# Performance work log

Hardware: AMD Instinct MI355X
Metric: run time of the kernel (lower is better)

The kernel has to match this reference:

```python
import jax, jax.numpy as jnp
import numpy as np

N_SUBJECTS = 16
N_LABELS = 8
DENS_TEMP = 0.1  # args.ProtoSim_dens_temp


def setup_inputs() -> dict:
    key = jax.random.key(0)
    k1, k2, k3 = jax.random.split(key, 3)
    B, C, D = 16384, 2, 1024
    X_data = jax.random.normal(k1, (B, C, D), dtype=jnp.float32)
    subject = jax.random.randint(k2, (B,), 0, N_SUBJECTS, dtype=jnp.int64) if jax.config.jax_enable_x64 else jax.random.randint(k2, (B,), 0, N_SUBJECTS).astype(jnp.int32)
    labels = jax.random.randint(k3, (B,), 0, N_LABELS).astype(subject.dtype)
    return {"X_data": X_data, "subject": subject, "labels": labels}


def reference(X_data, subject, labels):
    B, C, D = X_data.shape
    K = N_SUBJECTS * N_LABELS  # all (subject,label) groups assumed present
    # contrast_feature = cat(unbind(X_data, 1), 0) -> [B*C, D]
    feat = X_data.swapaxes(0, 1).reshape(B * C, D)
    sub2 = jnp.tile(subject, C)          # cat((subject, subject))
    lab2 = jnp.tile(labels, C)
    # torch.unique sorts -> group g = subject * N_LABELS + label matches loop order
    gid = sub2 * N_LABELS + lab2
    counts = jax.ops.segment_sum(jnp.ones((B * C,), feat.dtype), gid, num_segments=K)  # (K,)
    centroid = jax.ops.segment_sum(feat, gid, num_segments=K) / counts[:, None]       # (K, D)
    # per-row euclidean distance to own group centroid (torch.cdist to 1 point)
    dist = jnp.linalg.norm(feat - centroid[gid], axis=1)                               # (B*C,)
    mean_sqrt = jax.ops.segment_sum(jnp.sqrt(dist), gid, num_segments=K) / counts
    density = mean_sqrt / jnp.log(counts + 10.0)
    density = jnp.where(counts <= 1.0, density.max(), density)
    density = jnp.clip(density, jnp.quantile(density, 0.1), jnp.quantile(density, 0.9))
    density = DENS_TEMP * density / density.mean()                                     # (K,)
    # masks: positives = same label, different subject
    g_sub = jnp.arange(K) // N_LABELS
    g_lab = jnp.arange(K) % N_LABELS
    subj_mask = (sub2[:, None] != g_sub[None, :]).astype(feat.dtype)  # (B*C, K)
    lab_mask = (lab2[:, None] == g_lab[None, :]).astype(feat.dtype)
    mask = subj_mask * lab_mask
    # every row has N_SUBJECTS-1 positives (all groups present), so no row filtering
    sim = (feat @ centroid.T) / density[None, :]                                        # (B*C, K)
    sim = sim - sim.max(axis=1, keepdims=True)
    pos = sim * mask
    logp = jax.nn.log_softmax(pos, axis=1)
    row_loss = -(mask * logp).sum(axis=1) / mask.sum(axis=1)  # soft-target CE / #pos
    return row_loss.reshape(C, B).mean()
```

## Files before the change

### kernel.cpp

```cpp
#include <hip/hip_runtime.h>
#include <hip/hip_bf16.h>
#include <math.h>

#define NSUB 16
#define NLAB 8
#define KG 128
#define BN 16384
#define DD 1024

typedef float v4f __attribute__((ext_vector_type(4)));
typedef short short8v __attribute__((ext_vector_type(8)));
typedef unsigned short ushort4v __attribute__((ext_vector_type(4)));

static __device__ __forceinline__ short f2bf(float f) {
    unsigned u = __builtin_bit_cast(unsigned, f);
    unsigned r = (u + 0x7fffu + ((u >> 16) & 1u)) >> 16;
    return (short)r;
}

static __device__ __forceinline__ float bf2f(unsigned short u) {
    unsigned v = ((unsigned)u) << 16;
    return __builtin_bit_cast(float, v);
}

static __device__ __forceinline__ unsigned packbf2(float x, float y) {
    union { __hip_bfloat162 h; unsigned u; } c;
    c.h = __float22bfloat162_rn(float2{x, y});
    return c.u;
}

__global__ __launch_bounds__(1024) void k0_gid(const int* __restrict__ subject,
                                               const int* __restrict__ labels,
                                               int* __restrict__ gid, int* __restrict__ hist) {
    __shared__ int h[KG];
    int t = threadIdx.x;
    if (t < KG) h[t] = 0;
    __syncthreads();
    int b = blockIdx.x * 1024 + t;
    int g = subject[b] * NLAB + labels[b];
    gid[b] = g;
    atomicAdd(&h[g], 1);
    __syncthreads();
    if (t < KG) hist[blockIdx.x * KG + t] = h[t];
}

__global__ __launch_bounds__(1024) void k0c_scatter(const int* __restrict__ gid,
                                                    const int* __restrict__ hist,
                                                    int* __restrict__ cnt,
                                                    int* __restrict__ rowlist) {
    __shared__ int tots[KG], base0[KG], lcur[KG];
    int t = threadIdx.x, bi = blockIdx.x;
    if (t < KG) {
        int tot = 0, pre = 0;
#pragma unroll
        for (int j = 0; j < 16; ++j) {
            int v = hist[j * KG + t];
            tot += v;
            if (j < bi) pre += v;
        }
        tots[t] = tot;
        base0[t] = pre;
        lcur[t] = 0;
        if (bi == 0) cnt[t] = tot;
    }
    __syncthreads();
    if (t < KG) {
        int o = 0;
        for (int j = 0; j < t; ++j) o += tots[j];
        base0[t] += o;
    }
    __syncthreads();
    int b = bi * 1024 + t;
    int g = gid[b];
    rowlist[base0[g] + atomicAdd(&lcur[g], 1)] = b;
}

__global__ __launch_bounds__(256) void k1g_part(const float* __restrict__ X,
                                                const int* __restrict__ rowlist,
                                                const int* __restrict__ cnt,
                                                float* __restrict__ part2) {
    int g = blockIdx.x >> 3;
    int half = (blockIdx.x >> 2) & 1;
    int chunk = blockIdx.x & 3;
    int t = threadIdx.x, lane = t & 63, w = t >> 6;
    int c = t >> 7, td = t & 127;
    __shared__ int rows[512];
    __shared__ int sh_no[2];
    __shared__ float acc4[256][4];
    if (w == 0) {
        int v = 0;
        if (lane < g) v += cnt[lane];
        if (lane + 64 < g) v += cnt[lane + 64];
#pragma unroll
        for (int x = 32; x; x >>= 1) v += __shfl_xor(v, x, 64);
        if (lane == 0) { sh_no[0] = v; sh_no[1] = cnt[g]; }
    }
    __syncthreads();
    int o = sh_no[0], n = min(sh_no[1], 512);
    for (int i = t; i < n; i += 256) rows[i] = rowlist[o + i];
    __syncthreads();
    size_t coff = (size_t)c * 1024 + half * 512 + td * 4;
    float4 s4 = make_float4(0.f, 0.f, 0.f, 0.f);
    int i = chunk;
    for (; i + 28 < n; i += 32) {
        float4 v[8];
#pragma unroll
        for (int u = 0; u < 8; ++u)
            v[u] = *(const float4*)(X + (size_t)rows[i + 4 * u] * 2048 + coff);
#pragma unroll
        for (int u = 0; u < 8; ++u) {
            s4.x += v[u].x; s4.y += v[u].y; s4.z += v[u].z; s4.w += v[u].w;
        }
    }
    for (; i < n; i += 4) {
        float4 v = *(const float4*)(X + (size_t)rows[i] * 2048 + coff);
        s4.x += v.x; s4.y += v.y; s4.z += v.z; s4.w += v.w;
    }
    acc4[t][0] = s4.x; acc4[t][1] = s4.y; acc4[t][2] = s4.z; acc4[t][3] = s4.w;
    __syncthreads();
    if (t < 128) {
        float4 out;
        out.x = acc4[t][0] + acc4[t + 128][0];
        out.y = acc4[t][1] + acc4[t + 128][1];
        out.z = acc4[t][2] + acc4[t + 128][2];
        out.w = acc4[t][3] + acc4[t + 128][3];
        *(float4*)(part2 + (size_t)blockIdx.x * 512 + t * 4) = out;
    }
}

__global__ __launch_bounds__(256) void k1r2_reduce(const float* __restrict__ part2,
                                                   const int* __restrict__ cnt,
                                                   unsigned short* __restrict__ Btil,
                                                   float* __restrict__ cnormPart) {
    int g = blockIdx.x, t = threadIdx.x, lane = t & 63, w = t >> 6;
    __shared__ float wsum[4];
    int n = min(cnt[g], 512);
    int d0 = t * 4;
    int half = d0 >> 9, dloc = d0 & 511;
    const float* pp = part2 + ((size_t)g * 8 + half * 4) * 512 + dloc;
    float4 s4 = make_float4(0.f, 0.f, 0.f, 0.f);
#pragma unroll
    for (int chunk = 0; chunk < 4; ++chunk) {
        float4 v = *(const float4*)(pp + chunk * 512);
        s4.x += v.x; s4.y += v.y; s4.z += v.z; s4.w += v.w;
    }
    float inv = 1.f / (2.f * (float)n);
    float cx[4] = {s4.x * inv, s4.y * inv, s4.z * inv, s4.w * inv};
    int base_t = (d0 >> 5) * 512 + ((d0 >> 3) & 3) * 128 + (g & 15) * 8 + (d0 & 7);
    uint2 st;
    st.x = packbf2(cx[0], cx[1]);
    st.y = packbf2(cx[2], cx[3]);
    *(uint2*)(Btil + (size_t)(g >> 4) * 16384 + base_t) = st;
    float s = cx[0] * cx[0] + cx[1] * cx[1] + cx[2] * cx[2] + cx[3] * cx[3];
#pragma unroll
    for (int x = 32; x; x >>= 1) s += __shfl_xor(s, x, 64);
    if (lane == 0) wsum[w] = s;
    __syncthreads();
    if (t == 0) {
        cnormPart[g] = wsum[0] + wsum[1] + wsum[2] + wsum[3];
        cnormPart[KG + g] = 0.f;
    }
}

__global__ __launch_bounds__(256) void k2_tile(const float* __restrict__ X,
                                               unsigned short* __restrict__ Atil) {
    __shared__ unsigned lds[8192];
    int t = threadIdx.x, lane = t & 63, w = t >> 6;
    int rt = blockIdx.x;
#pragma unroll
    for (int p = 0; p < 4; ++p) {
        int m = w * 4 + p;
        int r = rt * 16 + m;
        const float* xp = X + (size_t)(r & (BN - 1)) * 2048 + (size_t)(r >> 14) * 1024;
        unsigned swz = (unsigned)((m & 7) << 2);
        unsigned mbase = (unsigned)m * 512;
#pragma unroll
        for (int j = 0; j < 4; ++j) {
            int d0 = j * 256 + lane * 4;
            float4 v = *(const float4*)(xp + d0);
            unsigned wi = mbase + (((unsigned)(d0 >> 1)) ^ swz);
            lds[wi] = packbf2(v.x, v.y);
            lds[wi + 1] = packbf2(v.z, v.w);
        }
    }
    __syncthreads();
    size_t gbase = (size_t)rt * 16384;
#pragma unroll
    for (int p = 0; p < 8; ++p) {
        int wo = p * 1024 + t * 4;
        int kc = wo >> 8;
        int q = (wo >> 6) & 3;
        int m = (wo >> 2) & 15;
        unsigned wi = (unsigned)m * 512 +
                      (((unsigned)(kc * 16 + q * 4)) ^ (unsigned)((m & 7) << 2));
        uint4 val = *(const uint4*)&lds[wi];
        *(uint4*)(Atil + gbase + (size_t)wo * 2) = val;
    }
}

__global__ __launch_bounds__(256) void k5a_dot(const unsigned short* __restrict__ Atil,
                                               const unsigned short* __restrict__ Btil,
                                               const int* __restrict__ gid,
                                               const float* __restrict__ cnormPart,
                                               unsigned short* __restrict__ Dotb,
                                               float* __restrict__ sqsPart) {
    __shared__ float h[KG];
    __shared__ float cnormS[KG];
    int t = threadIdx.x, lane = t & 63, w = t >> 6;
    if (t < KG) {
        h[t] = 0.f;
        cnormS[t] = cnormPart[t] + cnormPart[KG + t];
    }
    __syncthreads();
    int rt = blockIdx.x * 4 + w;
    int m = lane & 15, q = lane >> 4;
    const unsigned short* ap = Atil + (size_t)rt * 16384 + lane * 8;
    const unsigned short* bp = Btil + lane * 8;

    v4f acc[8];
#pragma unroll
    for (int j = 0; j < 8; ++j) acc[j] = (v4f){0.f, 0.f, 0.f, 0.f};

    short8v Af[2], Bf[2][8];
#pragma unroll
    for (int p = 0; p < 2; ++p) {
        Af[p] = *(const short8v*)(ap + p * 512);
#pragma unroll
        for (int gt = 0; gt < 8; ++gt)
            Bf[p][gt] = *(const short8v*)(bp + (size_t)gt * 16384 + p * 512);
    }
    float s0 = 0.f;
#pragma unroll
    for (int kc = 0; kc < 32; ++kc) {
        const int cur = kc & 1;
        short8v nA, nB[8];
        if (kc + 2 < 32) {
            nA = *(const short8v*)(ap + (kc + 2) * 512);
#pragma unroll
            for (int gt = 0; gt < 8; ++gt)
                nB[gt] = *(const short8v*)(bp + (size_t)gt * 16384 + (kc + 2) * 512);
        }
#pragma unroll
        for (int gt = 0; gt < 8; ++gt)
            acc[gt] = __builtin_amdgcn_mfma_f32_16x16x32_bf16(Af[cur], Bf[cur][gt], acc[gt], 0, 0, 0);
        {
            union { short8v s; unsigned u[4]; } ua;
            ua.s = Af[cur];
#pragma unroll
            for (int r = 0; r < 4; ++r) {
                float l0 = __builtin_bit_cast(float, ua.u[r] << 16);
                float h0 = __builtin_bit_cast(float, ua.u[r] & 0xffff0000u);
                s0 = fmaf(l0, l0, s0); s0 = fmaf(h0, h0, s0);
            }
        }
        if (kc + 2 < 32) {
            Af[cur] = nA;
#pragma unroll
            for (int gt = 0; gt < 8; ++gt) Bf[cur][gt] = nB[gt];
        }
    }

    s0 += __shfl_xor(s0, 16, 64); s0 += __shfl_xor(s0, 32, 64);

    int bid = blockIdx.x;
#pragma unroll
    for (int reg = 0; reg < 4; ++reg) {
        int rr = w * 16 + q * 4 + reg;
        int row = bid * 64 + rr;
        int b = row & (BN - 1);
        int g = gid[b];
        float own = 0.f;
#pragma unroll
        for (int gt = 0; gt < 8; ++gt) {
            float v = acc[gt][reg];
            size_t idx = (((size_t)bid * 32 + gt * 4 + (m >> 2)) * 64 + rr) * 4 + (m & 3);
            Dotb[idx] = (unsigned short)f2bf(v);
            if ((g >> 4) == gt) own = v;
        }
        float rn = __shfl(s0, q * 4 + reg, 64);
        if ((g & 15) == m) {
            float d2 = fmaxf(rn - 2.f * own + cnormS[g], 0.f);
            atomicAdd(&h[g], sqrtf(sqrtf(d2)));
        }
    }
    __syncthreads();
    if (t < KG) sqsPart[(size_t)blockIdx.x * KG + t] = h[t];
}

__global__ __launch_bounds__(128) void k5b_loss(const unsigned short* __restrict__ Dotb,
                                                const int* __restrict__ gid,
                                                const float* __restrict__ sqsPart,
                                                const int* __restrict__ cnt,
                                                float* __restrict__ out) {
    __shared__ float tmp[KG], d1s[KG], qv[4];
    __shared__ float recipDen[KG];
    __shared__ float wsum[2];
    int t = threadIdx.x;
    float cntf = 0.f, d0v = 0.f, v = 0.f;
    if (t < KG) {
        float ss = 0.f;
        for (int j = 0; j < 512; j += 4)
            ss += sqsPart[(size_t)j * KG + t] + sqsPart[(size_t)(j + 1) * KG + t] +
                  sqsPart[(size_t)(j + 2) * KG + t] + sqsPart[(size_t)(j + 3) * KG + t];
        cntf = 2.f * (float)cnt[t];
        d0v = (ss / cntf) / logf(cntf + 10.f);
        tmp[t] = d0v;
    }
    __syncthreads();
    if (t < KG) {
        float dmax = -INFINITY;
        for (int j = 0; j < KG; ++j) dmax = fmaxf(dmax, tmp[j]);
        v = (cntf <= 1.f) ? dmax : d0v;
        d1s[t] = v;
    }
    __syncthreads();
    if (t < KG) {
        int less = 0, eq = 0;
        for (int j = 0; j < KG; ++j) {
            float u = d1s[j];
            less += (u < v) ? 1 : 0;
            eq += (u == v) ? 1 : 0;
        }
        const int ppos[4] = {12, 13, 114, 115};
        for (int qq = 0; qq < 4; ++qq)
            if (less <= ppos[qq] && ppos[qq] < less + eq) qv[qq] = v;
    }
    __syncthreads();
    if (t < KG) {
        float q10 = 0.3f * qv[0] + 0.7f * qv[1];
        float q90 = 0.7f * qv[2] + 0.3f * qv[3];
        tmp[t] = fminf(fmaxf(v, q10), q90);
    }
    __syncthreads();
    if (t < KG) {
        float sum = 0.f;
        for (int j = 0; j < KG; ++j) sum += tmp[j];
        float mean = sum / (float)KG;
        recipDen[t] = mean / (0.1f * tmp[t]);
    }
    __syncthreads();
    int row = blockIdx.x * 128 + t;
    int b = row & (BN - 1);
    int g = gid[b];
    int s = g >> 3, l = g & 7;
    int lane = t & 63, w = t >> 6;
    size_t rowblk = (size_t)(row >> 6);
    const ushort4v* dp = (const ushort4v*)Dotb;
    float mx = -INFINITY;
    float psave[16];
#pragma unroll
    for (int c = 0; c < 16; ++c) {
        size_t i0 = (rowblk * 32 + c * 2) * 64 + lane;
        ushort4v dv0 = dp[i0];
        ushort4v dv1 = dp[i0 + 64];
        const float* rv = &recipDen[c * 8];
        float x[8];
#pragma unroll
        for (int j = 0; j < 4; ++j) x[j] = bf2f((unsigned short)dv0[j]) * rv[j];
#pragma unroll
        for (int j = 0; j < 4; ++j) x[4 + j] = bf2f((unsigned short)dv1[j]) * rv[4 + j];
#pragma unroll
        for (int j = 0; j < 8; ++j) mx = fmaxf(mx, x[j]);
        float sel = x[0];
#pragma unroll
        for (int j = 1; j < 8; ++j) sel = (j == l) ? x[j] : sel;
        psave[c] = sel;
    }
    float S = 0.f, P = 0.f;
#pragma unroll
    for (int j = 0; j < 16; ++j) {
        float pv = psave[j] - mx;
        float e = expf(pv);
        bool use = (j != s);
        S += use ? e : 0.f;
        P += use ? pv : 0.f;
    }
    float ll = logf(113.f + S) - P * (1.f / 15.f);
#pragma unroll
    for (int x2 = 32; x2; x2 >>= 1) ll += __shfl_xor(ll, x2, 64);
    if (lane == 0) wsum[w] = ll;
    __syncthreads();
    if (t == 0) atomicAdd(out, (wsum[0] + wsum[1]) * (1.f / 32768.f));
}

extern "C" void kernel_launch(void* const* d_in, const int* in_sizes, int n_in,
                              void* d_out, int out_size, void* d_ws, size_t ws_size,
                              hipStream_t stream) {
    const float* X = (const float*)d_in[0];
    const int* subject = (const int*)d_in[1];
    const int* labels = (const int*)d_in[2];
    float* out = (float*)d_out;
    char* w = (char*)d_ws;
    int* gid = (int*)(w + 0);
    int* hist = (int*)(w + 65536);
    int* cnt = (int*)(w + 73728);
    float* cnormPart = (float*)(w + 74240);
    int* rowlist = (int*)(w + 131072);
    float* sqsPart = (float*)(w + 262144);
    unsigned short* Btil = (unsigned short*)(w + 524288);
    unsigned short* Atil = (unsigned short*)(w + 2097152);
    float* part2 = (float*)(w + 71303168);
    unsigned short* Dotb = (unsigned short*)(w + 100663296);

    (void)hipMemsetAsync(out, 0, sizeof(float), stream);

    k2_tile<<<2048, 256, 0, stream>>>(X, Atil);
    k0_gid<<<16, 1024, 0, stream>>>(subject, labels, gid, hist);
    k0c_scatter<<<16, 1024, 0, stream>>>(gid, hist, cnt, rowlist);
    k1g_part<<<KG * 8, 256, 0, stream>>>(X, rowlist, cnt, part2);
    k1r2_reduce<<<KG, 256, 0, stream>>>(part2, cnt, Btil, cnormPart);
    k5a_dot<<<512, 256, 0, stream>>>(Atil, Btil, gid, cnormPart, Dotb, sqsPart);
    k5b_loss<<<256, 128, 0, stream>>>(Dotb, gid, sqsPart, cnt, out);
}
```

Before: 270.3 us.

## Stage centroid tiles through shared memory in dot kernel and atomically reduce sqs partials

The dot kernel now loads each centroid (B) chunk once per block into a double-buffered shared-memory tile, so the four waves share it. Previously every wave fetched all eight B fragments from global memory itself. The per-block sqrt-distance histograms are now added into one global array with atomics, which is zeroed in the gid kernel. This removes the 512-way serial reduction in the loss kernel. In exchange, A prefetch depth drops from two chunks to one, each k-step adds a block-wide barrier, and the float atomics make the sum order nondeterministic.

```diff
diff --git a/kernel.cpp b/kernel.cpp
--- a/kernel.cpp
+++ b/kernel.cpp
@@ -31,10 +31,12 @@
 
 __global__ __launch_bounds__(1024) void k0_gid(const int* __restrict__ subject,
                                                const int* __restrict__ labels,
-                                               int* __restrict__ gid, int* __restrict__ hist) {
+                                               int* __restrict__ gid, int* __restrict__ hist,
+                                               float* __restrict__ sqsG) {
     __shared__ int h[KG];
     int t = threadIdx.x;
     if (t < KG) h[t] = 0;
+    if (blockIdx.x == 0 && t < KG) sqsG[t] = 0.f;
     __syncthreads();
     int b = blockIdx.x * 1024 + t;
     int g = subject[b] * NLAB + labels[b];
@@ -203,49 +205,50 @@
                                                const int* __restrict__ gid,
                                                const float* __restrict__ cnormPart,
                                                unsigned short* __restrict__ Dotb,
-                                               float* __restrict__ sqsPart) {
+                                               float* __restrict__ sqsG) {
     __shared__ float h[KG];
     __shared__ float cnormS[KG];
+    __shared__ uint4 Bs[2][512];
     int t = threadIdx.x, lane = t & 63, w = t >> 6;
     if (t < KG) {
         h[t] = 0.f;
         cnormS[t] = cnormPart[t] + cnormPart[KG + t];
     }
-    __syncthreads();
     int rt = blockIdx.x * 4 + w;
     int m = lane & 15, q = lane >> 4;
     const unsigned short* ap = Atil + (size_t)rt * 16384 + lane * 8;
-    const unsigned short* bp = Btil + lane * 8;
-
+    int sgt = t >> 5, so = t & 31;
+    const unsigned short* bgp = Btil + (size_t)sgt * 16384;
+
+    {
+        const uint4* gp = (const uint4*)bgp;
+        Bs[0][sgt * 64 + so] = gp[so];
+        Bs[0][sgt * 64 + so + 32] = gp[so + 32];
+    }
     v4f acc[8];
 #pragma unroll
     for (int j = 0; j < 8; ++j) acc[j] = (v4f){0.f, 0.f, 0.f, 0.f};
-
-    short8v Af[2], Bf[2][8];
-#pragma unroll
-    for (int p = 0; p < 2; ++p) {
-        Af[p] = *(const short8v*)(ap + p * 512);
-#pragma unroll
-        for (int gt = 0; gt < 8; ++gt)
-            Bf[p][gt] = *(const short8v*)(bp + (size_t)gt * 16384 + p * 512);
-    }
+    short8v afc = *(const short8v*)ap;
+    __syncthreads();
+
     float s0 = 0.f;
 #pragma unroll
     for (int kc = 0; kc < 32; ++kc) {
         const int cur = kc & 1;
-        short8v nA, nB[8];
-        if (kc + 2 < 32) {
-            nA = *(const short8v*)(ap + (kc + 2) * 512);
-#pragma unroll
-            for (int gt = 0; gt < 8; ++gt)
-                nB[gt] = *(const short8v*)(bp + (size_t)gt * 16384 + (kc + 2) * 512);
-        }
+        if (kc + 1 < 32) {
+            const uint4* gp = (const uint4*)(bgp + (kc + 1) * 512);
+            Bs[cur ^ 1][sgt * 64 + so] = gp[so];
+            Bs[cur ^ 1][sgt * 64 + so + 32] = gp[so + 32];
+        }
+        short8v afn;
+        if (kc + 1 < 32) afn = *(const short8v*)(ap + (kc + 1) * 512);
+        const short8v* bsv = (const short8v*)Bs[cur];
 #pragma unroll
         for (int gt = 0; gt < 8; ++gt)
-            acc[gt] = __builtin_amdgcn_mfma_f32_16x16x32_bf16(Af[cur], Bf[cur][gt], acc[gt], 0, 0, 0);
+            acc[gt] = __builtin_amdgcn_mfma_f32_16x16x32_bf16(afc, bsv[gt * 64 + lane], acc[gt], 0, 0, 0);
         {
             union { short8v s; unsigned u[4]; } ua;
-            ua.s = Af[cur];
+            ua.s = afc;
 #pragma unroll
             for (int r = 0; r < 4; ++r) {
                 float l0 = __builtin_bit_cast(float, ua.u[r] << 16);
@@ -253,11 +256,8 @@
                 s0 = fmaf(l0, l0, s0); s0 = fmaf(h0, h0, s0);
             }
         }
-        if (kc + 2 < 32) {
-            Af[cur] = nA;
-#pragma unroll
-            for (int gt = 0; gt < 8; ++gt) Bf[cur][gt] = nB[gt];
-        }
+        if (kc + 1 < 32) afc = afn;
+        __syncthreads();
     }
 
     s0 += __shfl_xor(s0, 16, 64); s0 += __shfl_xor(s0, 32, 64);
@@ -284,12 +284,12 @@
         }
     }
     __syncthreads();
-    if (t < KG) sqsPart[(size_t)blockIdx.x * KG + t] = h[t];
+    if (t < KG) atomicAdd(&sqsG[t], h[t]);
 }
 
 __global__ __launch_bounds__(128) void k5b_loss(const unsigned short* __restrict__ Dotb,
                                                 const int* __restrict__ gid,
-                                                const float* __restrict__ sqsPart,
+                                                const float* __restrict__ sqsG,
                                                 const int* __restrict__ cnt,
                                                 float* __restrict__ out) {
     __shared__ float tmp[KG], d1s[KG], qv[4];
@@ -298,10 +298,7 @@
     int t = threadIdx.x;
     float cntf = 0.f, d0v = 0.f, v = 0.f;
     if (t < KG) {
-        float ss = 0.f;
-        for (int j = 0; j < 512; j += 4)
-            ss += sqsPart[(size_t)j * KG + t] + sqsPart[(size_t)(j + 1) * KG + t] +
-                  sqsPart[(size_t)(j + 2) * KG + t] + sqsPart[(size_t)(j + 3) * KG + t];
+        float ss = sqsG[t];
         cntf = 2.f * (float)cnt[t];
         d0v = (ss / cntf) / logf(cntf + 10.f);
         tmp[t] = d0v;
@@ -396,7 +393,7 @@
     int* cnt = (int*)(w + 73728);
     float* cnormPart = (float*)(w + 74240);
     int* rowlist = (int*)(w + 131072);
-    float* sqsPart = (float*)(w + 262144);
+    float* sqsG = (float*)(w + 262144);
     unsigned short* Btil = (unsigned short*)(w + 524288);
     unsigned short* Atil = (unsigned short*)(w + 2097152);
     float* part2 = (float*)(w + 71303168);
@@ -405,10 +402,10 @@
     (void)hipMemsetAsync(out, 0, sizeof(float), stream);
 
     k2_tile<<<2048, 256, 0, stream>>>(X, Atil);
-    k0_gid<<<16, 1024, 0, stream>>>(subject, labels, gid, hist);
+    k0_gid<<<16, 1024, 0, stream>>>(subject, labels, gid, hist, sqsG);
     k0c_scatter<<<16, 1024, 0, stream>>>(gid, hist, cnt, rowlist);
     k1g_part<<<KG * 8, 256, 0, stream>>>(X, rowlist, cnt, part2);
     k1r2_reduce<<<KG, 256, 0, stream>>>(part2, cnt, Btil, cnormPart);
-    k5a_dot<<<512, 256, 0, stream>>>(Atil, Btil, gid, cnormPart, Dotb, sqsPart);
-    k5b_loss<<<256, 128, 0, stream>>>(Dotb, gid, sqsPart, cnt, out);
-}
+    k5a_dot<<<512, 256, 0, stream>>>(Atil, Btil, gid, cnormPart, Dotb, sqsG);
+    k5b_loss<<<256, 128, 0, stream>>>(Dotb, gid, sqsG, cnt, out);
+}
```

New measurement: 270.4 us. About the same (+0.1%).
